# Kernel optimization log

Measured on AMD Instinct MI355X. Metric: run time of the kernel, lower is better.

## Reference

```python
import jax, jax.numpy as jnp
import numpy as np

B, S, D, H, K = 16, 4096, 256, 512, 3
EPS = 1e-5


def setup_inputs() -> dict:
    key = jax.random.key(0)
    ks = jax.random.split(key, 16)
    glorot = lambda k, shape: jax.random.uniform(
        k, shape, jnp.float32, -1.0, 1.0) * np.sqrt(6.0 / (shape[0] + shape[-1]))
    return {
        "inputs": jax.random.normal(ks[0], (B, S, D), jnp.float32),
        "mask": jax.random.randint(ks[1], (B, S), 0, 2, jnp.int32),
        "in_w": glorot(ks[2], (H, D)),
        "in_b": jnp.zeros((H,), jnp.float32),
        "gate_w": glorot(ks[3], (H, D)),
        "gate_b": jnp.zeros((H,), jnp.float32),
        "dw_w": glorot(ks[4], (H, 1, K)),
        "dw_b": jnp.zeros((H,), jnp.float32),
        "pw_w": glorot(ks[5], (H, H, 1)),
        "pw_b": jnp.zeros((H,), jnp.float32),
        "ln_g": jnp.ones((H,), jnp.float32),
        "ln_b": jnp.zeros((H,), jnp.float32),
        "A_log": jax.random.normal(ks[6], (H,), jnp.float32) * -0.1,
        "Bp": jax.random.normal(ks[7], (H,), jnp.float32) * 0.1,
        "Cp": jax.random.normal(ks[8], (H,), jnp.float32) * 0.1,
    }


def _forward(inputs, mask, in_w, in_b, gate_w, gate_b, dw_w, dw_b,
             pw_w, pw_b, ln_g, ln_b, A_log, Bp, Cp):
    # projections: torch Linear is x @ W.T + b
    x_lin = jnp.einsum('bsd,hd->bsh', inputs, in_w) + in_b
    g_lin = jnp.einsum('bsd,hd->bsh', inputs, gate_w) + gate_b
    h = jnp.tanh(x_lin)
    m_f = mask.astype(h.dtype)                      # [B,S]
    h = h * m_f[:, :, None]
    # depthwise conv over time: [B,H,S] with groups=H, 'same' padding
    pad = (K - 1) // 2
    h_t = jnp.transpose(h, (0, 2, 1))               # [B,H,S]
    h_conv = jax.lax.conv_general_dilated(
        h_t, dw_w, window_strides=(1,), padding=[(pad, pad)],
        dimension_numbers=('NCH', 'OIH', 'NCH'), feature_group_count=H)
    h_conv = h_conv + dw_b[None, :, None]
    h_conv = jnp.transpose(h_conv, (0, 2, 1))       # [B,S,H]
    # pointwise 1x1 conv
    h_conv = jnp.einsum('bsh,oh->bso', h_conv, pw_w[:, :, 0]) + pw_b
    u = jax.nn.silu(h_conv + h)
    g = jax.nn.sigmoid(g_lin)
    a_exp = jnp.exp(-jax.nn.softplus(A_log))        # [H]

    def step(carry, xs):
        state, last = carry
        ut, gt, mt = xs                             # [B,H],[B,H],[B]
        new_state = gt * (a_exp * state) + (1.0 - gt) * (Bp * ut)
        keep = (mt > 0.5)[:, None]
        state = jnp.where(keep, new_state, state)
        y = state * Cp
        last = jnp.where(keep, y, last)
        return (state, last), last

    init = (jnp.zeros((B, H), u.dtype), jnp.zeros((B, H), u.dtype))
    xs = (jnp.transpose(u, (1, 0, 2)), jnp.transpose(g, (1, 0, 2)),
          jnp.transpose(m_f, (1, 0)))
    _, y_seq = jax.lax.scan(step, init, xs)         # [S,B,H]
    y_seq = jnp.transpose(y_seq, (1, 0, 2))         # [B,S,H]
    # LayerNorm over last dim
    mu = jnp.mean(y_seq, axis=-1, keepdims=True)
    var = jnp.var(y_seq, axis=-1, keepdims=True)
    return (y_seq - mu) * jax.lax.rsqrt(var + EPS) * ln_g + ln_b


def reference(inputs, mask, in_w, in_b, gate_w, gate_b, dw_w, dw_b,
              pw_w, pw_b, ln_g, ln_b, A_log, Bp, Cp):
    return _forward(inputs, mask, in_w, in_b, gate_w, gate_b, dw_w, dw_b,
                    pw_w, pw_b, ln_g, ln_b, A_log, Bp, Cp)
```

## Files before the change

### kernel.cpp

```cpp
#include <hip/hip_runtime.h>
#include <hip/hip_bf16.h>
#include <math.h>

#define B_  16
#define S_  4096
#define D_  256
#define H_  512
#define BS_ 65536
#define BSH_ 33554432L
#define BSD_ 16777216L
#define CCH 128
#define LCH 32
#define TPAD 136

typedef __bf16 bf16;
typedef __bf16 bf16x8 __attribute__((ext_vector_type(8)));
typedef float  f32x4  __attribute__((ext_vector_type(4)));

#define AS1 __attribute__((address_space(1)))
#define AS3 __attribute__((address_space(3)))

__device__ __forceinline__ void gload_lds16(const void* g, void* l) {
  __builtin_amdgcn_global_load_lds((const AS1 void*)g, (AS3 void*)l, 16, 0, 0);
}

#if __has_builtin(__builtin_amdgcn_exp2f)
#define EXP2F __builtin_amdgcn_exp2f
#else
#define EXP2F exp2f
#endif
#if __has_builtin(__builtin_amdgcn_rcpf)
#define RCPF __builtin_amdgcn_rcpf
#else
#define RCPF(x) (1.f/(x))
#endif
#define L2E 1.4426950408889634f

__device__ __forceinline__ float fsigmoid(float x) {
  return RCPF(1.f + EXP2F(-L2E * x));
}
__device__ __forceinline__ float ftanh(float x) {
  return 2.f * RCPF(1.f + EXP2F(-2.f * L2E * x)) - 1.f;
}
__device__ __forceinline__ float fsilu(float x) {
  return x * RCPF(1.f + EXP2F(-L2E * x));
}

__global__ void k_cast_x(const float* __restrict__ x, bf16* __restrict__ xb, int n8) {
  int i = blockIdx.x * blockDim.x + threadIdx.x;
  if (i >= n8) return;
  const float4* p = (const float4*)x + (long)i * 2;
  float4 a = p[0], b = p[1];
  bf16x8 o;
  o[0]=(bf16)a.x; o[1]=(bf16)a.y; o[2]=(bf16)a.z; o[3]=(bf16)a.w;
  o[4]=(bf16)b.x; o[5]=(bf16)b.y; o[6]=(bf16)b.z; o[7]=(bf16)b.w;
  ((bf16x8*)xb)[i] = o;
}

__global__ void k_cast_w(const float* __restrict__ in_w, const float* __restrict__ gate_w,
                         const float* __restrict__ pw_w,
                         bf16* __restrict__ w1, bf16* __restrict__ pw) {
  int i = blockIdx.x * blockDim.x + threadIdx.x;
  const int HD = H_ * D_;
  if (i < HD)            w1[i] = (bf16)in_w[i];
  else if (i < 2 * HD)   w1[i] = (bf16)gate_w[i - HD];
  else {
    int j = i - 2 * HD;
    if (j < H_ * H_)     pw[j] = (bf16)pw_w[j];
  }
}

template<int KDIM, int EPI>
__global__ __launch_bounds__(256)
void k_gemm(const bf16* __restrict__ A, const bf16* __restrict__ Bw,
            const int* __restrict__ mask,
            const float* __restrict__ bias0, const float* __restrict__ bias1,
            const bf16* __restrict__ hbuf,
            bf16* __restrict__ out0, bf16* __restrict__ out1, int Ntiles)
{
  extern __shared__ char smem_raw[];
  bf16* Asm = (bf16*)smem_raw;
  bf16* Bsm = (bf16*)(smem_raw + 8192);
  bf16* tile = (bf16*)smem_raw;

  const int t = threadIdx.x;
  const int w = t >> 6, lane = t & 63;
  const int nwg = gridDim.x;
  const int wg = (blockIdx.x & 7) * (nwg >> 3) + (blockIdx.x >> 3);
  const int bn0 = (wg % Ntiles) * 128;
  const int bm0 = (wg / Ntiles) * 128;
  const int wm = w >> 1, wn = w & 1;
  const int srow = t >> 2;
  const int skoff = (t & 3) * 8;
  const int fr = lane & 15, kq = lane >> 4;

  f32x4 acc[4][4];
#pragma unroll
  for (int i = 0; i < 4; ++i)
#pragma unroll
    for (int j = 0; j < 4; ++j) acc[i][j] = (f32x4){0.f, 0.f, 0.f, 0.f};

  for (int k0 = 0; k0 < KDIM; k0 += 32) {
#pragma unroll
    for (int i = 0; i < 2; ++i) {
      gload_lds16(A  + (long)(bm0 + i * 64 + srow) * KDIM + k0 + skoff,
                  Asm + i * 2048 + w * 512 + lane * 8);
      gload_lds16(Bw + (long)(bn0 + i * 64 + srow) * KDIM + k0 + skoff,
                  Bsm + i * 2048 + w * 512 + lane * 8);
    }
    __syncthreads();
    bf16x8 af[4], bfr[4];
#pragma unroll
    for (int mi = 0; mi < 4; ++mi)
      af[mi] = *(const bf16x8*)&Asm[(wm * 64 + mi * 16 + fr) * 32 + kq * 8];
#pragma unroll
    for (int ni = 0; ni < 4; ++ni)
      bfr[ni] = *(const bf16x8*)&Bsm[(wn * 64 + ni * 16 + fr) * 32 + kq * 8];
#pragma unroll
    for (int mi = 0; mi < 4; ++mi)
#pragma unroll
      for (int ni = 0; ni < 4; ++ni)
        acc[mi][ni] = __builtin_amdgcn_mfma_f32_16x16x32_bf16(af[mi], bfr[ni], acc[mi][ni], 0, 0, 0);
    __syncthreads();
  }

  const bool hside = (EPI != 1) || (bn0 < H_);
#pragma unroll
  for (int mi = 0; mi < 4; ++mi) {
#pragma unroll
    for (int rr = 0; rr < 4; ++rr) {
      const int row = wm * 64 + mi * 16 + kq * 4 + rr;
      const int gm = bm0 + row;
      float mf = 1.f;
      if (EPI == 1) mf = (mask[gm] != 0) ? 1.f : 0.f;
#pragma unroll
      for (int ni = 0; ni < 4; ++ni) {
        const int col = wn * 64 + ni * 16 + fr;
        float c = acc[mi][ni][rr];
        float val;
        if (EPI == 1) {
          const int gn = bn0 + col;
          val = hside ? ftanh(c + bias0[gn]) * mf
                      : fsigmoid(c + bias1[gn - H_]);
        } else {
          val = c + bias0[bn0 + col];
        }
        tile[row * TPAD + col] = (bf16)val;
      }
    }
  }
  __syncthreads();

  const int pr = t >> 4;
  const int pc = (t & 15) * 8;
#pragma unroll
  for (int rr = 0; rr < 8; ++rr) {
    const int row = pr + rr * 16;
    const long gm = bm0 + row;
    bf16x8 v = *(const bf16x8*)&tile[row * TPAD + pc];
    if (EPI == 1) {
      if (hside) *(bf16x8*)&out0[gm * H_ + bn0 + pc] = v;
      else       *(bf16x8*)&out1[gm * H_ + (bn0 - H_) + pc] = v;
    } else {
      bf16x8 hb = *(const bf16x8*)&hbuf[gm * H_ + bn0 + pc];
      bf16x8 o;
#pragma unroll
      for (int k = 0; k < 8; ++k) {
        float s = (float)v[k] + (float)hb[k];
        o[k] = (bf16)fsilu(s);
      }
      *(bf16x8*)&out0[gm * H_ + bn0 + pc] = o;
    }
  }
}

__global__ void k_dwconv(const bf16* __restrict__ h, const float* __restrict__ dww,
                         const float* __restrict__ dwb, bf16* __restrict__ hc)
{
  long idx = (long)blockIdx.x * blockDim.x + threadIdx.x;
  long m = idx >> 6;
  int h8 = ((int)idx & 63) << 3;
  int s = (int)(m & (S_ - 1));
  bf16x8 c0, c1, c2;
#pragma unroll
  for (int j = 0; j < 8; ++j) { c0[j] = (bf16)0.f; c2[j] = (bf16)0.f; }
  if (s > 0)        c0 = *(const bf16x8*)(h + (m - 1) * H_ + h8);
  c1 = *(const bf16x8*)(h + m * H_ + h8);
  if (s < S_ - 1)   c2 = *(const bf16x8*)(h + (m + 1) * H_ + h8);
  bf16x8 o;
#pragma unroll
  for (int j = 0; j < 8; ++j) {
    int hh = h8 + j;
    float v = (float)c0[j] * dww[hh * 3 + 0] + (float)c1[j] * dww[hh * 3 + 1]
            + (float)c2[j] * dww[hh * 3 + 2] + dwb[hh];
    o[j] = (bf16)v;
  }
  *(bf16x8*)(hc + m * H_ + h8) = o;
}


__global__ __launch_bounds__(512)
void k_scan1(const bf16* __restrict__ u, const bf16* __restrict__ g,
             const int* __restrict__ mask, const float* __restrict__ A_log,
             const float* __restrict__ Bp,
             float* __restrict__ Ac, float* __restrict__ Bc)
{
  int c = blockIdx.x, b = blockIdx.y, h = threadIdx.x;
  float aexp = 1.f / (1.f + expf(A_log[h]));
  float bp = Bp[h];
  float At = 1.f, Bt = 0.f;
  long base = ((long)b * S_ + (long)c * LCH) * H_ + h;
  const int* mrow = mask + b * S_ + c * LCH;
  for (int sl = 0; sl < LCH; ++sl) {
    float uv = (float)u[base + (long)sl * H_];
    float gv = (float)g[base + (long)sl * H_];
    bool mm = mrow[sl] != 0;
    float a_s = mm ? gv * aexp : 1.f;
    float b_s = mm ? (1.f - gv) * (bp * uv) : 0.f;
    At = a_s * At;
    Bt = fmaf(a_s, Bt, b_s);
  }
  long o = ((long)c * B_ + b) * H_ + h;
  Ac[o] = At; Bc[o] = Bt;
}

__global__ __launch_bounds__(256)
void k_scan2(const float* __restrict__ Ac, const float* __restrict__ Bc,
             float* __restrict__ Sin)
{
  int tid = blockIdx.x * 256 + threadIdx.x;
  int b = tid >> 9, h = tid & (H_ - 1);
  float st = 0.f;
  for (int c = 0; c < CCH; ++c) {
    long o = ((long)c * B_ + b) * H_ + h;
    Sin[o] = st;
    st = fmaf(Ac[o], st, Bc[o]);
  }
}

__global__ __launch_bounds__(512)
void k_scan3(const bf16* __restrict__ u, const bf16* __restrict__ g,
             const int* __restrict__ mask, const float* __restrict__ A_log,
             const float* __restrict__ Bp, const float* __restrict__ Cp,
             const float* __restrict__ Sin,
             const float* __restrict__ ln_g, const float* __restrict__ ln_b,
             float* __restrict__ out)
{
  __shared__ float ylds[LCH][H_];
  int c = blockIdx.x, b = blockIdx.y, h = threadIdx.x;
  float aexp = 1.f / (1.f + expf(A_log[h]));
  float bp = Bp[h], cp = Cp[h];
  float st = Sin[((long)c * B_ + b) * H_ + h];
  long base = ((long)b * S_ + (long)c * LCH) * H_ + h;
  const int* mrow = mask + b * S_ + c * LCH;
  for (int sl = 0; sl < LCH; ++sl) {
    float uv = (float)u[base + (long)sl * H_];
    float gv = (float)g[base + (long)sl * H_];
    bool mm = mrow[sl] != 0;
    float a_s = mm ? gv * aexp : 1.f;
    float b_s = mm ? (1.f - gv) * (bp * uv) : 0.f;
    st = fmaf(a_s, st, b_s);
    ylds[sl][h] = st * cp;
  }
  __syncthreads();
  int wv = h >> 6, ln = h & 63;
#pragma unroll
  for (int rr = 0; rr < 4; ++rr) {
    int row = wv * 4 + rr;
    float v[8];
    float sum = 0.f, sq = 0.f;
#pragma unroll
    for (int j = 0; j < 8; ++j) {
      v[j] = ylds[row][ln + 64 * j];
      sum += v[j]; sq += v[j] * v[j];
    }
#pragma unroll
    for (int off = 32; off; off >>= 1) {
      sum += __shfl_xor(sum, off);
      sq  += __shfl_xor(sq, off);
    }
    float mu = sum * (1.f / H_);
    float var = sq * (1.f / H_) - mu * mu;
    float rs = rsqrtf(var + 1e-5f);
    long ob = ((long)b * S_ + (long)c * LCH + row) * H_;
#pragma unroll
    for (int j = 0; j < 8; ++j) {
      int col = ln + 64 * j;
      out[ob + col] = (v[j] - mu) * rs * ln_g[col] + ln_b[col];
    }
  }
}

extern "C" void kernel_launch(void* const* d_in, const int* in_sizes, int n_in,
                              void* d_out, int out_size, void* d_ws, size_t ws_size,
                              hipStream_t stream)
{
  const float* x      = (const float*)d_in[0];
  const int*   mask   = (const int*)d_in[1];
  const float* in_w   = (const float*)d_in[2];
  const float* in_b   = (const float*)d_in[3];
  const float* gate_w = (const float*)d_in[4];
  const float* gate_b = (const float*)d_in[5];
  const float* dw_w   = (const float*)d_in[6];
  const float* dw_b   = (const float*)d_in[7];
  const float* pw_w   = (const float*)d_in[8];
  const float* pw_b   = (const float*)d_in[9];
  const float* ln_g   = (const float*)d_in[10];
  const float* ln_b   = (const float*)d_in[11];
  const float* A_log  = (const float*)d_in[12];
  const float* Bp     = (const float*)d_in[13];
  const float* Cp     = (const float*)d_in[14];

  char* ws = (char*)d_ws;
  bf16*  xb  = (bf16*)(ws + 0L);
  bf16*  h   = (bf16*)(ws + 33554432L);
  bf16*  hc  = (bf16*)(ws + 100663296L);
  bf16*  u   = (bf16*)(ws + 167772160L);
  bf16*  g   = (bf16*)(ws + 234881024L);
  bf16*  w1  = (bf16*)(ws + 301989888L);
  bf16*  pw  = (bf16*)(ws + 302514176L);
  float* Ac  = (float*)(ws + 303038464L);
  float* Bc  = (float*)(ws + 307232768L);
  float* Sin = (float*)(ws + 311427072L);
  float* out = (float*)d_out;

  const int gemm_lds = 128 * TPAD * 2;

  k_cast_x<<<8192, 256, 0, stream>>>(x, xb, (int)(BSD_ / 8));
  k_cast_w<<<2048, 256, 0, stream>>>(in_w, gate_w, pw_w, w1, pw);
  k_gemm<256, 1><<<512 * 8, 256, gemm_lds, stream>>>(xb, w1, mask, in_b, gate_b, nullptr, h, g, 8);
  k_dwconv<<<16384, 256, 0, stream>>>(h, dw_w, dw_b, hc);
  k_gemm<512, 2><<<512 * 4, 256, gemm_lds, stream>>>(hc, pw, nullptr, pw_b, nullptr, h, u, nullptr, 4);
  k_scan1<<<dim3(CCH, B_), 512, 0, stream>>>(u, g, mask, A_log, Bp, Ac, Bc);
  k_scan2<<<32, 256, 0, stream>>>(Ac, Bc, Sin);
  k_scan3<<<dim3(CCH, B_), 512, 0, stream>>>(u, g, mask, A_log, Bp, Cp, Sin, ln_g, ln_b, out);
}
```

Before: 370.5 us.

## Double-buffer GEMM LDS tiles and prefetch chunk carries in scan2

The GEMM K-loop now keeps two LDS buffers. The next 32-wide K slice is issued via global_load_lds while the MFMAs run on the current slice, which cuts the barriers per iteration from two to one. The chunk-combine scan also loads the next chunk's A/B coefficients before using the current ones, to hide global load latency in its serial loop. The change doubles the GEMM's LDS footprint to 32KB. That only works if the dynamic shared memory at launch was sized to match, and it may lower occupancy.

```diff
diff --git a/kernel.cpp b/kernel.cpp
--- a/kernel.cpp
+++ b/kernel.cpp
@@ -79,8 +79,8 @@
             bf16* __restrict__ out0, bf16* __restrict__ out1, int Ntiles)
 {
   extern __shared__ char smem_raw[];
-  bf16* Asm = (bf16*)smem_raw;
-  bf16* Bsm = (bf16*)(smem_raw + 8192);
+  bf16* As_ = (bf16*)smem_raw;
+  bf16* Bs_ = (bf16*)smem_raw + 8192;
   bf16* tile = (bf16*)smem_raw;
 
   const int t = threadIdx.x;
@@ -100,29 +100,44 @@
 #pragma unroll
     for (int j = 0; j < 4; ++j) acc[i][j] = (f32x4){0.f, 0.f, 0.f, 0.f};
 
+#pragma unroll
+  for (int i = 0; i < 2; ++i) {
+    gload_lds16(A  + (long)(bm0 + i * 64 + srow) * KDIM + skoff,
+                As_ + i * 2048 + t * 8);
+    gload_lds16(Bw + (long)(bn0 + i * 64 + srow) * KDIM + skoff,
+                Bs_ + i * 2048 + t * 8);
+  }
+
+  int cur = 0;
   for (int k0 = 0; k0 < KDIM; k0 += 32) {
-#pragma unroll
-    for (int i = 0; i < 2; ++i) {
-      gload_lds16(A  + (long)(bm0 + i * 64 + srow) * KDIM + k0 + skoff,
-                  Asm + i * 2048 + w * 512 + lane * 8);
-      gload_lds16(Bw + (long)(bn0 + i * 64 + srow) * KDIM + k0 + skoff,
-                  Bsm + i * 2048 + w * 512 + lane * 8);
-    }
     __syncthreads();
+    if (k0 + 32 < KDIM) {
+      const int nxt = cur ^ 1;
+#pragma unroll
+      for (int i = 0; i < 2; ++i) {
+        gload_lds16(A  + (long)(bm0 + i * 64 + srow) * KDIM + (k0 + 32) + skoff,
+                    As_ + nxt * 4096 + i * 2048 + t * 8);
+        gload_lds16(Bw + (long)(bn0 + i * 64 + srow) * KDIM + (k0 + 32) + skoff,
+                    Bs_ + nxt * 4096 + i * 2048 + t * 8);
+      }
+    }
+    const bf16* As = As_ + cur * 4096;
+    const bf16* Bs = Bs_ + cur * 4096;
     bf16x8 af[4], bfr[4];
 #pragma unroll
     for (int mi = 0; mi < 4; ++mi)
-      af[mi] = *(const bf16x8*)&Asm[(wm * 64 + mi * 16 + fr) * 32 + kq * 8];
+      af[mi] = *(const bf16x8*)&As[(wm * 64 + mi * 16 + fr) * 32 + kq * 8];
 #pragma unroll
     for (int ni = 0; ni < 4; ++ni)
-      bfr[ni] = *(const bf16x8*)&Bsm[(wn * 64 + ni * 16 + fr) * 32 + kq * 8];
+      bfr[ni] = *(const bf16x8*)&Bs[(wn * 64 + ni * 16 + fr) * 32 + kq * 8];
 #pragma unroll
     for (int mi = 0; mi < 4; ++mi)
 #pragma unroll
       for (int ni = 0; ni < 4; ++ni)
         acc[mi][ni] = __builtin_amdgcn_mfma_f32_16x16x32_bf16(af[mi], bfr[ni], acc[mi][ni], 0, 0, 0);
-    __syncthreads();
-  }
+    cur ^= 1;
+  }
+  __syncthreads();
 
   const bool hside = (EPI != 1) || (bn0 < H_);
 #pragma unroll
@@ -230,11 +245,16 @@
 {
   int tid = blockIdx.x * 256 + threadIdx.x;
   int b = tid >> 9, h = tid & (H_ - 1);
+  const long stride = (long)B_ * H_;
+  long o = (long)b * H_ + h;
   float st = 0.f;
+  float a = Ac[o], bb = Bc[o];
   for (int c = 0; c < CCH; ++c) {
-    long o = ((long)c * B_ + b) * H_ + h;
+    float an = 0.f, bn = 0.f;
+    if (c + 1 < CCH) { an = Ac[o + stride]; bn = Bc[o + stride]; }
     Sin[o] = st;
-    st = fmaf(Ac[o], st, Bc[o]);
+    st = fmaf(a, st, bb);
+    a = an; bb = bn; o += stride;
   }
 }
 
```

After: 383.7 us. +3.6%, slower.
